# Performance work log

Hardware: AMD Instinct MI355X
Metric: run time of the kernel (lower is better)

The kernel has to match this reference:

```python
import jax, jax.numpy as jnp
import numpy as np

B, T, D, H, C = 8, 1024, 1024, 16, 8  # batch, seq, d_model, heads, num_concepts
DK = D // H
LAMBD = 5.0


def setup_inputs() -> dict:
    key = jax.random.key(0)
    ks = jax.random.split(key, 14)
    s = 0.02
    return {
        "qa_concept": jax.random.normal(ks[0], (B, T, T, C), jnp.float32),
        "query": jax.random.normal(ks[1], (B, T, D), jnp.float32),
        "key": jax.random.normal(ks[2], (B, T, D), jnp.float32),
        "value": jax.random.normal(ks[3], (B, T, D), jnp.float32),
        "Wq": jax.random.normal(ks[4], (D, D), jnp.float32) * s,
        "bq": jnp.zeros((D,), jnp.float32),
        "Wk": jax.random.normal(ks[5], (D, D), jnp.float32) * s,
        "bk": jnp.zeros((D,), jnp.float32),
        "Wv": jax.random.normal(ks[6], (D, D), jnp.float32) * s,
        "bv": jnp.zeros((D,), jnp.float32),
        "Wo": jax.random.normal(ks[7], (D, D), jnp.float32) * s,
        "bo": jnp.zeros((D,), jnp.float32),
        "mask": jax.random.randint(ks[8], (B, T), 0, 2, jnp.int32),
    }


def reference(qa_concept, query, key, value, Wq, bq, Wk, bk, Wv, bv, Wo, bo, mask):
    # Linear projections (torch Linear: y = x @ W.T + b)
    q = (query @ Wq.T + bq).reshape(B, T, H, DK).transpose(0, 2, 1, 3)  # [B,H,T,dk]
    k = (key @ Wk.T + bk).reshape(B, T, H, DK).transpose(0, 2, 1, 3)
    v = (value @ Wv.T + bv).reshape(B, T, H, DK).transpose(0, 2, 1, 3)
    scores = jnp.einsum("bhqd,bhkd->bhqk", q, k) / jnp.sqrt(jnp.float32(DK))
    # concept bias added to first C heads only
    bias = LAMBD * jnp.transpose(qa_concept, (0, 3, 1, 2))  # [B,C,T,T]
    scores = scores.at[:, :C, :, :].add(bias)
    # mask: [B,T] -> [B,1,1,T], fill -1e9 where 0
    scores = jnp.where(mask[:, None, None, :] == 0, jnp.float32(-1e9), scores)
    attn = jax.nn.softmax(scores, axis=-1)  # dropout is identity in eval
    x = jnp.einsum("bhqk,bhkd->bhqd", attn, v)
    x = x.transpose(0, 2, 1, 3).reshape(B, T, D)
    return x @ Wo.T + bo
```

## Files before the change

kernel.cpp:

```cpp
#include <hip/hip_runtime.h>

#define B_  8
#define T_  1024
#define D_  1024
#define H_  16
#define DK_ 64
#define C_  8
#define N_  (B_*T_)

typedef __attribute__((ext_vector_type(8))) short bf16x8;
typedef __attribute__((ext_vector_type(4))) float f32x4;
typedef __attribute__((ext_vector_type(8))) unsigned short u16x8;
typedef __attribute__((ext_vector_type(4))) unsigned short u16x4;

__device__ __forceinline__ float bf2f(unsigned short u) {
  union { unsigned int i; float f; } x; x.i = ((unsigned int)u) << 16; return x.f;
}
__device__ __forceinline__ unsigned short f2bf(float f) {
  union { float f; unsigned int i; } x; x.f = f;
  unsigned int r = (x.i + 0x7fffu + ((x.i >> 16) & 1u)) >> 16;
  return (unsigned short)r;
}
__device__ __forceinline__ unsigned short f2h(float f) {
  union { _Float16 h; unsigned short u; } x; x.h = (_Float16)f; return x.u;
}
__device__ __forceinline__ float h2f(unsigned short u) {
  union { _Float16 h; unsigned short u; } x; x.u = u; return (float)x.h;
}

__device__ __forceinline__ void gl_lds16(const unsigned short* g, unsigned short* l) {
  __builtin_amdgcn_global_load_lds(
      (const __attribute__((address_space(1))) unsigned int*)g,
      (__attribute__((address_space(3))) unsigned int*)l,
      16, 0, 0);
}

__global__ __launch_bounds__(256) void cvt32to16(
    const float* __restrict__ in, unsigned short* __restrict__ out, int n4) {
  int tid = blockIdx.x * blockDim.x + threadIdx.x;
  int stride = gridDim.x * blockDim.x;
  const float4* in4 = (const float4*)in;
  u16x4* out4 = (u16x4*)out;
  for (int i = tid; i < n4; i += stride) {
    float4 v = in4[i];
    u16x4 o = { f2bf(v.x), f2bf(v.y), f2bf(v.z), f2bf(v.w) };
    out4[i] = o;
  }
}

__global__ __launch_bounds__(256) void transposeQa(
    const float* __restrict__ qa, unsigned short* __restrict__ qat) {
  int b = blockIdx.x >> 10, q = blockIdx.x & 1023;
  int t = threadIdx.x;
  __shared__ float L[8][132];
  const float* src = qa + ((size_t)(b*T_ + q))*T_*C_;
  for (int ch = 0; ch < 8; ++ch) {
    int k0 = ch*128;
    float4 v = *(const float4*)(src + (size_t)(k0 + (t>>1))*C_ + (t&1)*4);
    int c4 = (t&1)*4, kk = t>>1;
    L[c4+0][kk] = v.x; L[c4+1][kk] = v.y; L[c4+2][kk] = v.z; L[c4+3][kk] = v.w;
    __syncthreads();
    int c = t >> 5, kk2 = (t&31)*4;
    float4 p = *(const float4*)&L[c][kk2];
    u16x4 o = { f2h(p.x), f2h(p.y), f2h(p.z), f2h(p.w) };
    *(u16x4*)(qat + ((size_t)(b*C_ + c)*T_ + q)*T_ + k0 + kk2) = o;
    __syncthreads();
  }
}

__global__ __launch_bounds__(256) void transposeV(
    const unsigned short* __restrict__ V, unsigned short* __restrict__ Vt) {
  int bid = blockIdx.x;
  int tt = bid & 15;
  int bh = bid >> 4;
  int b = bh >> 4, h = bh & 15;
  __shared__ unsigned short L[64][72];
  int r  = threadIdx.x >> 3;
  int c8 = (threadIdx.x & 7) * 8;
  const unsigned short* src = V + ((size_t)(b*T_ + tt*64))*D_ + h*64;
#pragma unroll
  for (int p = 0; p < 2; ++p) {
    int rr = r + p*32;
    u16x8 v = *(const u16x8*)(src + (size_t)rr*D_ + c8);
    *(u16x8*)&L[rr][c8] = v;
  }
  __syncthreads();
  unsigned short* dst = Vt + ((size_t)bh*64)*T_ + tt*64;
#pragma unroll
  for (int p = 0; p < 2; ++p) {
    int d = r + p*32;
    u16x8 o;
#pragma unroll
    for (int i = 0; i < 8; ++i) o[i] = L[c8 + i][d];
    *(u16x8*)(dst + (size_t)d*T_ + c8) = o;
  }
}

template <bool OUT_F32>
__global__ __launch_bounds__(256) void gemm_lds(
    const unsigned short* __restrict__ X, const unsigned short* __restrict__ W,
    const float* __restrict__ bias, void* __restrict__ Yv) {
  __shared__ __align__(16) unsigned short As[128*32];
  __shared__ __align__(16) unsigned short Bs[128*32];
  int orig = (blockIdx.x & 7) * 64 + (blockIdx.x >> 3);
  int bm = orig >> 3, bn = orig & 7;
  int t = threadIdx.x, lane = t & 63, w = t >> 6;
  int wr = w >> 1, wc = w & 1;
  int r16 = lane & 15, kg = lane >> 4;

  int srow0 = lane >> 2;
  int scol  = (lane & 3) * 8;
  const unsigned short* Ab = X + (size_t)(bm*128)*D_ + scol;
  const unsigned short* Bb = W + (size_t)(bn*128)*D_ + scol;

  f32x4 acc[4][4];
#pragma unroll
  for (int m = 0; m < 4; ++m)
#pragma unroll
    for (int n = 0; n < 4; ++n) acc[m][n] = (f32x4){0.f,0.f,0.f,0.f};

  for (int k0 = 0; k0 < D_; k0 += 32) {
    __syncthreads();
#pragma unroll
    for (int c = 0; c < 2; ++c) {
      int cidx = w*2 + c;
      int row = cidx*16 + srow0;
      gl_lds16(Ab + (size_t)row*D_ + k0, As + cidx*512);
      gl_lds16(Bb + (size_t)row*D_ + k0, Bs + cidx*512);
    }
    __syncthreads();

    bf16x8 a[4], bb[4];
#pragma unroll
    for (int m = 0; m < 4; ++m)
      a[m] = *(const bf16x8*)(As + (wr*64 + m*16 + r16)*32 + kg*8);
#pragma unroll
    for (int n = 0; n < 4; ++n)
      bb[n] = *(const bf16x8*)(Bs + (wc*64 + n*16 + r16)*32 + kg*8);
#pragma unroll
    for (int m = 0; m < 4; ++m)
#pragma unroll
      for (int n = 0; n < 4; ++n)
        acc[m][n] = __builtin_amdgcn_mfma_f32_16x16x32_bf16(a[m], bb[n], acc[m][n], 0, 0, 0);
  }

#pragma unroll
  for (int n = 0; n < 4; ++n) {
    int col = bn*128 + wc*64 + n*16 + r16;
    float bv = bias[col];
#pragma unroll
    for (int m = 0; m < 4; ++m) {
      int row0 = bm*128 + wr*64 + m*16 + kg*4;
#pragma unroll
      for (int jj = 0; jj < 4; ++jj) {
        float rv = acc[m][n][jj] + bv;
        if constexpr (OUT_F32)
          ((float*)Yv)[(size_t)(row0 + jj)*D_ + col] = rv;
        else
          ((unsigned short*)Yv)[(size_t)(row0 + jj)*D_ + col] = f2bf(rv);
      }
    }
  }
}

__global__ __launch_bounds__(256, 3) void attn4b(
    const unsigned short* __restrict__ Q, const unsigned short* __restrict__ K,
    const unsigned short* __restrict__ Vt, const unsigned short* __restrict__ qat,
    const int* __restrict__ mask, unsigned short* __restrict__ X) {
  int swzid = ((blockIdx.x & 7) << 7) | (blockIdx.x >> 3);
  int qt = swzid & 7, h = (swzid >> 3) & 15, b = swzid >> 7;
  int w = threadIdx.x >> 6, lane = threadIdx.x & 63;
  int r16 = lane & 15, kg = lane >> 4;
  int q0w = qt*128 + w*32;
  int bh = b*H_ + h;

  __shared__ unsigned short Ks[2][64][64];
  __shared__ unsigned short Vs[2][64][64];
  __shared__ unsigned int  P32[4][2][16][32];

  int rl = lane >> 3;
  int eo = ((lane & 7) * 8) ^ (rl << 3);
  const unsigned short* Kb = K + ((size_t)b*T_)*D_ + h*DK_;
  const unsigned short* Vb = Vt + ((size_t)bh*DK_)*T_;

  int sw16 = (r16 & 7) << 4;
  int ko0 = ((kg*16 +  0) ^ sw16) >> 1;
  int ko1 = ((kg*16 + 64) ^ sw16) >> 1;
  int sw32 = (r16 & 7) << 2;

  bf16x8 qfr[2][2];
#pragma unroll
  for (int qf = 0; qf < 2; ++qf) {
    const unsigned short* qrow = Q + ((size_t)b*T_ + q0w + qf*16 + r16)*D_ + h*DK_ + kg*8;
    qfr[qf][0] = *(const bf16x8*)qrow;
    qfr[qf][1] = *(const bf16x8*)(qrow + 32);
  }

  f32x4 acc[2][4];
#pragma unroll
  for (int qf = 0; qf < 2; ++qf)
#pragma unroll
    for (int db = 0; db < 4; ++db) acc[qf][db] = (f32x4){0.f,0.f,0.f,0.f};
  float mold[2] = {-3e38f, -3e38f};
  float lpart[2] = {0.f, 0.f};

  const int* mrow = mask + b*T_;
  const unsigned short* qab0 = qat + ((size_t)((b*C_ + h)*T_) + q0w + r16)*T_;

#pragma unroll
  for (int c = 0; c < 2; ++c) {
    int cc = w*2 + c;
    gl_lds16(Kb + (size_t)(cc*8 + rl)*D_ + eo, &Ks[0][cc*8][0]);
    gl_lds16(Vb + (size_t)(cc*8 + rl)*T_ + eo, &Vs[0][cc*8][0]);
  }
  __syncthreads();

  for (int t = 0; t < 16; ++t) {
    int k0 = t*64, bb = t & 1;
    if (t < 15) {
      int kn = k0 + 64, nb = bb ^ 1;
#pragma unroll
      for (int c = 0; c < 2; ++c) {
        int cc = w*2 + c;
        gl_lds16(Kb + (size_t)(kn + cc*8 + rl)*D_ + eo, &Ks[nb][cc*8][0]);
        gl_lds16(Vb + (size_t)(cc*8 + rl)*T_ + kn + eo, &Vs[nb][cc*8][0]);
      }
    }
    u16x4 qv[2][4];
    if (h < C_) {
#pragma unroll
      for (int qf = 0; qf < 2; ++qf)
#pragma unroll
        for (int kt = 0; kt < 4; ++kt)
          qv[qf][kt] = *(const u16x4*)(qab0 + (size_t)qf*16*T_ + k0 + kt*16 + kg*4);
    }
    int mk = mrow[k0 + lane];
    unsigned long long bits = __ballot(mk != 0);

    f32x4 s[2][4];
#pragma unroll
    for (int kt = 0; kt < 4; ++kt) {
      bf16x8 kf0 = *(const bf16x8*)&Ks[bb][kt*16 + r16][ko0];
      bf16x8 kf1 = *(const bf16x8*)&Ks[bb][kt*16 + r16][ko1];
#pragma unroll
      for (int qf = 0; qf < 2; ++qf) {
        f32x4 z = (f32x4){0.f,0.f,0.f,0.f};
        z = __builtin_amdgcn_mfma_f32_16x16x32_bf16(kf0, qfr[qf][0], z, 0, 0, 0);
        z = __builtin_amdgcn_mfma_f32_16x16x32_bf16(kf1, qfr[qf][1], z, 0, 0, 0);
        s[qf][kt] = z;
      }
    }

    float pmaxq[2];
#pragma unroll
    for (int qf = 0; qf < 2; ++qf) {
      float pmax = -3e38f;
#pragma unroll
      for (int kt = 0; kt < 4; ++kt)
#pragma unroll
        for (int jj = 0; jj < 4; ++jj) {
          float v = s[qf][kt][jj] * 0.125f;
          if (h < C_) v += 5.0f * h2f(qv[qf][kt][jj]);
          int idx = kt*16 + kg*4 + jj;
          v = ((bits >> idx) & 1ULL) ? v : -1e9f;
          s[qf][kt][jj] = v;
          pmax = fmaxf(pmax, v);
        }
      pmax = fmaxf(pmax, __shfl_xor(pmax, 16, 64));
      pmax = fmaxf(pmax, __shfl_xor(pmax, 32, 64));
      pmaxq[qf] = pmax;
    }
    if (!__all(pmaxq[0] - mold[0] <= 8.0f && pmaxq[1] - mold[1] <= 8.0f)) {
#pragma unroll
      for (int qf = 0; qf < 2; ++qf) {
        float mnew = fmaxf(mold[qf], pmaxq[qf]);
        float sc = __expf(mold[qf] - mnew);
        mold[qf] = mnew;
        lpart[qf] *= sc;
        float scq[4];
#pragma unroll
        for (int jj = 0; jj < 4; ++jj) scq[jj] = __shfl(sc, kg*4 + jj, 64);
#pragma unroll
        for (int db = 0; db < 4; ++db)
#pragma unroll
          for (int jj = 0; jj < 4; ++jj) acc[qf][db][jj] *= scq[jj];
      }
    }
#pragma unroll
    for (int qf = 0; qf < 2; ++qf) {
      unsigned int pk[8];
#pragma unroll
      for (int kt = 0; kt < 4; ++kt) {
        float p0 = __expf(s[qf][kt][0] - mold[qf]), p1 = __expf(s[qf][kt][1] - mold[qf]);
        float p2 = __expf(s[qf][kt][2] - mold[qf]), p3 = __expf(s[qf][kt][3] - mold[qf]);
        lpart[qf] += (p0 + p1) + (p2 + p3);
        pk[kt*2+0] = (unsigned)f2bf(p0) | ((unsigned)f2bf(p1) << 16);
        pk[kt*2+1] = (unsigned)f2bf(p2) | ((unsigned)f2bf(p3) << 16);
      }
#pragma unroll
      for (int kt = 0; kt < 4; ++kt)
        *(uint2*)&P32[w][qf][r16][(kt*8 + kg*2) ^ sw32] =
            make_uint2(pk[kt*2], pk[kt*2+1]);
    }
    __builtin_amdgcn_sched_barrier(0);
    asm volatile("s_waitcnt lgkmcnt(0)");
    __builtin_amdgcn_sched_barrier(0);
#pragma unroll
    for (int qf = 0; qf < 2; ++qf) {
      bf16x8 pa0 = *(const bf16x8*)&P32[w][qf][r16][(kg*4) ^ sw32];
      bf16x8 pa1 = *(const bf16x8*)&P32[w][qf][r16][(16 + kg*4) ^ sw32];
#pragma unroll
      for (int db = 0; db < 4; ++db) {
        bf16x8 vf0 = *(const bf16x8*)&Vs[bb][db*16 + r16][ko0];
        bf16x8 vf1 = *(const bf16x8*)&Vs[bb][db*16 + r16][ko1];
        acc[qf][db] = __builtin_amdgcn_mfma_f32_16x16x32_bf16(pa0, vf0, acc[qf][db], 0, 0, 0);
        acc[qf][db] = __builtin_amdgcn_mfma_f32_16x16x32_bf16(pa1, vf1, acc[qf][db], 0, 0, 0);
      }
    }
    __syncthreads();
  }

#pragma unroll
  for (int qf = 0; qf < 2; ++qf) {
    float lp = lpart[qf];
    lp += __shfl_xor(lp, 16, 64);
    lp += __shfl_xor(lp, 32, 64);
    float linv = 1.0f / lp;
    float invq[4];
#pragma unroll
    for (int jj = 0; jj < 4; ++jj) invq[jj] = __shfl(linv, kg*4 + jj, 64);
#pragma unroll
    for (int jj = 0; jj < 4; ++jj)
#pragma unroll
      for (int db = 0; db < 4; ++db)
        X[((size_t)b*T_ + q0w + qf*16 + kg*4 + jj)*D_ + h*DK_ + db*16 + r16] =
            f2bf(acc[qf][db][jj] * invq[jj]);
  }
}

__global__ __launch_bounds__(256) void attn_fused(
    const unsigned short* __restrict__ Q, const unsigned short* __restrict__ K,
    const unsigned short* __restrict__ Vt, const float* __restrict__ qa,
    const int* __restrict__ mask, unsigned short* __restrict__ X) {
  int bid = blockIdx.x;
  int qt = bid & 15, h = (bid >> 4) & 15, b = bid >> 8;
  int w = threadIdx.x >> 6, lane = threadIdx.x & 63;
  int r16 = lane & 15, kg = lane >> 4;
  int q0 = qt*64 + w*16;
  int bh = b*H_ + h;

  __shared__ unsigned short P[4][16][72];

  const unsigned short* qrow = Q + ((size_t)b*T_ + q0 + r16)*D_ + h*DK_ + kg*8;
  bf16x8 qf0 = *(const bf16x8*)qrow;
  bf16x8 qf1 = *(const bf16x8*)(qrow + 32);

  f32x4 acc[4];
#pragma unroll
  for (int db = 0; db < 4; ++db) acc[db] = (f32x4){0.f,0.f,0.f,0.f};
  float mrow[4], lrow[4];
#pragma unroll
  for (int jj = 0; jj < 4; ++jj) { mrow[jj] = -3e38f; lrow[jj] = 0.f; }

  const int* mptr = mask + b*T_;
  const unsigned short* Kbase = K + ((size_t)b*T_)*D_ + h*DK_;
  const unsigned short* Vbase = Vt + ((size_t)bh*DK_)*T_;
  const float* qabase = qa + ((size_t)(b*T_ + q0 + kg*4))*T_*C_ + h;

  for (int k0 = 0; k0 < T_; k0 += 64) {
    f32x4 s[4];
#pragma unroll
    for (int kt = 0; kt < 4; ++kt) {
      const unsigned short* krow = Kbase + (size_t)(k0 + kt*16 + r16)*D_ + kg*8;
      f32x4 z = (f32x4){0.f,0.f,0.f,0.f};
      z = __builtin_amdgcn_mfma_f32_16x16x32_bf16(qf0, *(const bf16x8*)krow,        z, 0, 0, 0);
      z = __builtin_amdgcn_mfma_f32_16x16x32_bf16(qf1, *(const bf16x8*)(krow + 32), z, 0, 0, 0);
      s[kt] = z;
    }
    int mk[4];
#pragma unroll
    for (int kt = 0; kt < 4; ++kt) mk[kt] = mptr[k0 + kt*16 + r16];
    if (h < C_) {
#pragma unroll
      for (int kt = 0; kt < 4; ++kt)
#pragma unroll
        for (int jj = 0; jj < 4; ++jj) {
          float bb = qabase[(size_t)jj*T_*C_ + (size_t)(k0 + kt*16 + r16)*C_];
          s[kt][jj] = s[kt][jj]*0.125f + 5.0f*bb;
        }
    } else {
#pragma unroll
      for (int kt = 0; kt < 4; ++kt)
#pragma unroll
        for (int jj = 0; jj < 4; ++jj) s[kt][jj] *= 0.125f;
    }
#pragma unroll
    for (int kt = 0; kt < 4; ++kt)
#pragma unroll
      for (int jj = 0; jj < 4; ++jj)
        if (mk[kt] == 0) s[kt][jj] = -1e9f;

#pragma unroll
    for (int jj = 0; jj < 4; ++jj) {
      float v = fmaxf(fmaxf(s[0][jj], s[1][jj]), fmaxf(s[2][jj], s[3][jj]));
#pragma unroll
      for (int d = 1; d < 16; d <<= 1) v = fmaxf(v, __shfl_xor(v, d, 64));
      float mnew = fmaxf(mrow[jj], v);
      float sc = __expf(mrow[jj] - mnew);
      mrow[jj] = mnew;
      lrow[jj] *= sc;
#pragma unroll
      for (int db = 0; db < 4; ++db) acc[db][jj] *= sc;
      float rs = 0.f;
#pragma unroll
      for (int kt = 0; kt < 4; ++kt) {
        float p = __expf(s[kt][jj] - mnew);
        rs += p;
        P[w][kg*4 + jj][kt*16 + r16] = f2bf(p);
      }
#pragma unroll
      for (int d = 1; d < 16; d <<= 1) rs += __shfl_xor(rs, d, 64);
      lrow[jj] += rs;
    }
    __syncthreads();

    bf16x8 pa0 = *(const bf16x8*)&P[w][r16][kg*8];
    bf16x8 pa1 = *(const bf16x8*)&P[w][r16][32 + kg*8];
#pragma unroll
    for (int db = 0; db < 4; ++db) {
      const unsigned short* vr = Vbase + (size_t)(db*16 + r16)*T_ + k0 + kg*8;
      acc[db] = __builtin_amdgcn_mfma_f32_16x16x32_bf16(pa0, *(const bf16x8*)vr,        acc[db], 0, 0, 0);
      acc[db] = __builtin_amdgcn_mfma_f32_16x16x32_bf16(pa1, *(const bf16x8*)(vr + 32), acc[db], 0, 0, 0);
    }
  }

  float inv[4];
#pragma unroll
  for (int jj = 0; jj < 4; ++jj) inv[jj] = 1.0f / lrow[jj];
#pragma unroll
  for (int jj = 0; jj < 4; ++jj)
#pragma unroll
    for (int db = 0; db < 4; ++db)
      X[((size_t)b*T_ + q0 + kg*4 + jj)*D_ + h*DK_ + db*16 + r16] =
          f2bf(acc[db][jj] * inv[jj]);
}

extern "C" void kernel_launch(void* const* d_in, const int* in_sizes, int n_in,
                              void* d_out, int out_size, void* d_ws, size_t ws_size,
                              hipStream_t stream) {
  const float* qa    = (const float*)d_in[0];
  const float* query = (const float*)d_in[1];
  const float* key   = (const float*)d_in[2];
  const float* value = (const float*)d_in[3];
  const float* Wq = (const float*)d_in[4];
  const float* bq = (const float*)d_in[5];
  const float* Wk = (const float*)d_in[6];
  const float* bk = (const float*)d_in[7];
  const float* Wv = (const float*)d_in[8];
  const float* bv = (const float*)d_in[9];
  const float* Wo = (const float*)d_in[10];
  const float* bo = (const float*)d_in[11];
  const int* mask = (const int*)d_in[12];

  const size_t ND = (size_t)N_ * D_;
  const size_t DD = (size_t)D_ * D_;
  const size_t QAT = (size_t)B_ * C_ * T_ * T_;
  unsigned short* Qws = (unsigned short*)d_ws;
  unsigned short* Kws = Qws + ND;
  unsigned short* Vws = Kws + ND;
  unsigned short* Xws = Vws + ND;
  unsigned short* qbf = Xws + ND;
  unsigned short* kbf = qbf + ND;
  unsigned short* vbf = kbf + ND;
  unsigned short* wqbf = vbf + ND;
  unsigned short* wkbf = wqbf + DD;
  unsigned short* wvbf = wkbf + DD;
  unsigned short* wobf = wvbf + DD;
  unsigned short* qatws = wobf + DD;
  unsigned short* Vtws = qbf;

  bool fast = ws_size >= (7*ND + 4*DD + QAT) * sizeof(unsigned short);

  dim3 blk(256);
  cvt32to16<<<2048, blk, 0, stream>>>(query, qbf, (int)(ND/4));
  cvt32to16<<<2048, blk, 0, stream>>>(key,   kbf, (int)(ND/4));
  cvt32to16<<<2048, blk, 0, stream>>>(value, vbf, (int)(ND/4));
  cvt32to16<<<512,  blk, 0, stream>>>(Wq, wqbf, (int)(DD/4));
  cvt32to16<<<512,  blk, 0, stream>>>(Wk, wkbf, (int)(DD/4));
  cvt32to16<<<512,  blk, 0, stream>>>(Wv, wvbf, (int)(DD/4));
  cvt32to16<<<512,  blk, 0, stream>>>(Wo, wobf, (int)(DD/4));

  int ggrid = (N_/128) * (D_/128);
  gemm_lds<false><<<ggrid, blk, 0, stream>>>(qbf, wqbf, bq, Qws);
  gemm_lds<false><<<ggrid, blk, 0, stream>>>(kbf, wkbf, bk, Kws);
  gemm_lds<false><<<ggrid, blk, 0, stream>>>(vbf, wvbf, bv, Vws);

  transposeV<<<B_*H_*(T_/64), blk, 0, stream>>>(Vws, Vtws);

  if (fast) {
    transposeQa<<<B_*T_, blk, 0, stream>>>(qa, qatws);
    attn4b<<<B_*H_*(T_/128), blk, 0, stream>>>(Qws, Kws, Vtws, qatws, mask, Xws);
  } else {
    attn_fused<<<B_*H_*(T_/64), blk, 0, stream>>>(Qws, Kws, Vtws, qa, mask, Xws);
  }

  gemm_lds<true><<<ggrid, blk, 0, stream>>>(Xws, wobf, bo, (float*)d_out);
}
```

Before: 340.5 us.

## Batch conversion and QKV GEMM launches, prefetch concept bias and mask one tile ahead

After: 481.2 us. 41.3% more time.

```diff
diff --git a/kernel.cpp b/kernel.cpp
--- a/kernel.cpp
+++ b/kernel.cpp
@@ -35,15 +35,41 @@
       16, 0, 0);
 }
 
-__global__ __launch_bounds__(256) void cvt32to16(
-    const float* __restrict__ in, unsigned short* __restrict__ out, int n4) {
-  int tid = blockIdx.x * blockDim.x + threadIdx.x;
-  int stride = gridDim.x * blockDim.x;
+__global__ __launch_bounds__(256) void cvt_qkv(
+    const float* __restrict__ q, const float* __restrict__ k,
+    const float* __restrict__ v, unsigned short* __restrict__ qo,
+    unsigned short* __restrict__ ko, unsigned short* __restrict__ vo, int n4) {
+  int seg = blockIdx.x >> 10;
+  int bid = blockIdx.x & 1023;
+  const float* in = (seg == 0) ? q : (seg == 1) ? k : v;
+  unsigned short* out = (seg == 0) ? qo : (seg == 1) ? ko : vo;
+  int tid = bid * blockDim.x + threadIdx.x;
+  int stride = 1024 * 256;
   const float4* in4 = (const float4*)in;
   u16x4* out4 = (u16x4*)out;
   for (int i = tid; i < n4; i += stride) {
-    float4 v = in4[i];
-    u16x4 o = { f2bf(v.x), f2bf(v.y), f2bf(v.z), f2bf(v.w) };
+    float4 vv = in4[i];
+    u16x4 o = { f2bf(vv.x), f2bf(vv.y), f2bf(vv.z), f2bf(vv.w) };
+    out4[i] = o;
+  }
+}
+
+__global__ __launch_bounds__(256) void cvt_w(
+    const float* __restrict__ w0, const float* __restrict__ w1,
+    const float* __restrict__ w2, const float* __restrict__ w3,
+    unsigned short* __restrict__ o0, unsigned short* __restrict__ o1,
+    unsigned short* __restrict__ o2, unsigned short* __restrict__ o3, int n4) {
+  int seg = blockIdx.x >> 8;
+  int bid = blockIdx.x & 255;
+  const float* in = (seg == 0) ? w0 : (seg == 1) ? w1 : (seg == 2) ? w2 : w3;
+  unsigned short* out = (seg == 0) ? o0 : (seg == 1) ? o1 : (seg == 2) ? o2 : o3;
+  int tid = bid * blockDim.x + threadIdx.x;
+  int stride = 256 * 256;
+  const float4* in4 = (const float4*)in;
+  u16x4* out4 = (u16x4*)out;
+  for (int i = tid; i < n4; i += stride) {
+    float4 vv = in4[i];
+    u16x4 o = { f2bf(vv.x), f2bf(vv.y), f2bf(vv.z), f2bf(vv.w) };
     out4[i] = o;
   }
 }
@@ -97,12 +123,11 @@
 }
 
 template <bool OUT_F32>
-__global__ __launch_bounds__(256) void gemm_lds(
-    const unsigned short* __restrict__ X, const unsigned short* __restrict__ W,
-    const float* __restrict__ bias, void* __restrict__ Yv) {
-  __shared__ __align__(16) unsigned short As[128*32];
-  __shared__ __align__(16) unsigned short Bs[128*32];
-  int orig = (blockIdx.x & 7) * 64 + (blockIdx.x >> 3);
+__device__ __forceinline__ void gemm_body(
+    int blockid, const unsigned short* __restrict__ X,
+    const unsigned short* __restrict__ W, const float* __restrict__ bias,
+    void* __restrict__ Yv, unsigned short* As, unsigned short* Bs) {
+  int orig = (blockid & 7) * 64 + (blockid >> 3);
   int bm = orig >> 3, bn = orig & 7;
   int t = threadIdx.x, lane = t & 63, w = t >> 6;
   int wr = w >> 1, wc = w & 1;
@@ -163,7 +188,35 @@
   }
 }
 
-__global__ __launch_bounds__(256, 3) void attn4b(
+template <bool OUT_F32>
+__global__ __launch_bounds__(256) void gemm_lds(
+    const unsigned short* __restrict__ X, const unsigned short* __restrict__ W,
+    const float* __restrict__ bias, void* __restrict__ Yv) {
+  __shared__ __align__(16) unsigned short As[128*32];
+  __shared__ __align__(16) unsigned short Bs[128*32];
+  gemm_body<OUT_F32>(blockIdx.x, X, W, bias, Yv, As, Bs);
+}
+
+__global__ __launch_bounds__(256) void gemm_qkv(
+    const unsigned short* __restrict__ Xq, const unsigned short* __restrict__ Xk,
+    const unsigned short* __restrict__ Xv,
+    const unsigned short* __restrict__ Wq2, const unsigned short* __restrict__ Wk2,
+    const unsigned short* __restrict__ Wv2,
+    const float* __restrict__ bq2, const float* __restrict__ bk2,
+    const float* __restrict__ bv2,
+    unsigned short* __restrict__ Yq, unsigned short* __restrict__ Yk,
+    unsigned short* __restrict__ Yv2) {
+  __shared__ __align__(16) unsigned short As[128*32];
+  __shared__ __align__(16) unsigned short Bs[128*32];
+  int seg = blockIdx.x / 512, inner = blockIdx.x % 512;
+  const unsigned short* X = (seg == 0) ? Xq : (seg == 1) ? Xk : Xv;
+  const unsigned short* W = (seg == 0) ? Wq2 : (seg == 1) ? Wk2 : Wv2;
+  const float* bias = (seg == 0) ? bq2 : (seg == 1) ? bk2 : bv2;
+  unsigned short* Y = (seg == 0) ? Yq : (seg == 1) ? Yk : Yv2;
+  gemm_body<false>(inner, X, W, bias, Y, As, Bs);
+}
+
+__global__ __launch_bounds__(256, 3) void attn4c(
     const unsigned short* __restrict__ Q, const unsigned short* __restrict__ K,
     const unsigned short* __restrict__ Vt, const unsigned short* __restrict__ qat,
     const int* __restrict__ mask, unsigned short* __restrict__ X) {
@@ -213,12 +266,22 @@
     gl_lds16(Kb + (size_t)(cc*8 + rl)*D_ + eo, &Ks[0][cc*8][0]);
     gl_lds16(Vb + (size_t)(cc*8 + rl)*T_ + eo, &Vs[0][cc*8][0]);
   }
+  u16x4 qv_cur[2][4], qv_nxt[2][4];
+  if (h < C_) {
+#pragma unroll
+    for (int qf = 0; qf < 2; ++qf)
+#pragma unroll
+      for (int kt = 0; kt < 4; ++kt)
+        qv_cur[qf][kt] = *(const u16x4*)(qab0 + (size_t)qf*16*T_ + kt*16 + kg*4);
+  }
+  int mk_cur = mrow[lane], mk_nxt = 0;
   __syncthreads();
 
   for (int t = 0; t < 16; ++t) {
     int k0 = t*64, bb = t & 1;
+    int kn = (t < 15) ? (k0 + 64) : k0;
     if (t < 15) {
-      int kn = k0 + 64, nb = bb ^ 1;
+      int nb = bb ^ 1;
 #pragma unroll
       for (int c = 0; c < 2; ++c) {
         int cc = w*2 + c;
@@ -226,16 +289,15 @@
         gl_lds16(Vb + (size_t)(cc*8 + rl)*T_ + kn + eo, &Vs[nb][cc*8][0]);
       }
     }
-    u16x4 qv[2][4];
     if (h < C_) {
 #pragma unroll
       for (int qf = 0; qf < 2; ++qf)
 #pragma unroll
         for (int kt = 0; kt < 4; ++kt)
-          qv[qf][kt] = *(const u16x4*)(qab0 + (size_t)qf*16*T_ + k0 + kt*16 + kg*4);
-    }
-    int mk = mrow[k0 + lane];
-    unsigned long long bits = __ballot(mk != 0);
+          qv_nxt[qf][kt] = *(const u16x4*)(qab0 + (size_t)qf*16*T_ + kn + kt*16 + kg*4);
+    }
+    mk_nxt = mrow[kn + lane];
+    unsigned long long bits = __ballot(mk_cur != 0);
 
     f32x4 s[2][4];
 #pragma unroll
@@ -260,7 +322,7 @@
 #pragma unroll
         for (int jj = 0; jj < 4; ++jj) {
           float v = s[qf][kt][jj] * 0.125f;
-          if (h < C_) v += 5.0f * h2f(qv[qf][kt][jj]);
+          if (h < C_) v += 5.0f * h2f(qv_cur[qf][kt][jj]);
           int idx = kt*16 + kg*4 + jj;
           v = ((bits >> idx) & 1ULL) ? v : -1e9f;
           s[qf][kt][jj] = v;
@@ -317,6 +379,13 @@
         acc[qf][db] = __builtin_amdgcn_mfma_f32_16x16x32_bf16(pa1, vf1, acc[qf][db], 0, 0, 0);
       }
     }
+    if (h < C_) {
+#pragma unroll
+      for (int qf = 0; qf < 2; ++qf)
+#pragma unroll
+        for (int kt = 0; kt < 4; ++kt) qv_cur[qf][kt] = qv_nxt[qf][kt];
+    }
+    mk_cur = mk_nxt;
     __syncthreads();
   }
 
@@ -482,27 +551,20 @@
   bool fast = ws_size >= (7*ND + 4*DD + QAT) * sizeof(unsigned short);
 
   dim3 blk(256);
-  cvt32to16<<<2048, blk, 0, stream>>>(query, qbf, (int)(ND/4));
-  cvt32to16<<<2048, blk, 0, stream>>>(key,   kbf, (int)(ND/4));
-  cvt32to16<<<2048, blk, 0, stream>>>(value, vbf, (int)(ND/4));
-  cvt32to16<<<512,  blk, 0, stream>>>(Wq, wqbf, (int)(DD/4));
-  cvt32to16<<<512,  blk, 0, stream>>>(Wk, wkbf, (int)(DD/4));
-  cvt32to16<<<512,  blk, 0, stream>>>(Wv, wvbf, (int)(DD/4));
-  cvt32to16<<<512,  blk, 0, stream>>>(Wo, wobf, (int)(DD/4));
-
-  int ggrid = (N_/128) * (D_/128);
-  gemm_lds<false><<<ggrid, blk, 0, stream>>>(qbf, wqbf, bq, Qws);
-  gemm_lds<false><<<ggrid, blk, 0, stream>>>(kbf, wkbf, bk, Kws);
-  gemm_lds<false><<<ggrid, blk, 0, stream>>>(vbf, wvbf, bv, Vws);
+  cvt_qkv<<<3072, blk, 0, stream>>>(query, key, value, qbf, kbf, vbf, (int)(ND/4));
+  cvt_w<<<1024, blk, 0, stream>>>(Wq, Wk, Wv, Wo, wqbf, wkbf, wvbf, wobf, (int)(DD/4));
+
+  gemm_qkv<<<3*512, blk, 0, stream>>>(qbf, kbf, vbf, wqbf, wkbf, wvbf,
+                                      bq, bk, bv, Qws, Kws, Vws);
 
   transposeV<<<B_*H_*(T_/64), blk, 0, stream>>>(Vws, Vtws);
 
   if (fast) {
     transposeQa<<<B_*T_, blk, 0, stream>>>(qa, qatws);
-    attn4b<<<B_*H_*(T_/128), blk, 0, stream>>>(Qws, Kws, Vtws, qatws, mask, Xws);
+    attn4c<<<B_*H_*(T_/128), blk, 0, stream>>>(Qws, Kws, Vtws, qatws, mask, Xws);
   } else {
     attn_fused<<<B_*H_*(T_/64), blk, 0, stream>>>(Qws, Kws, Vtws, qa, mask, Xws);
   }
 
-  gemm_lds<true><<<ggrid, blk, 0, stream>>>(Xws, wobf, bo, (float*)d_out);
-}
+  gemm_lds<true><<<512, blk, 0, stream>>>(Xws, wobf, bo, (float*)d_out);
+}
```
